# Performance work log

Measured on AMD Instinct MI355X. Metric: run time of the kernel, lower is better.

The kernel has to match this reference:

```python
import jax, jax.numpy as jnp
import numpy as np

NUM_NODES = 16
HSZ = 512
BSZ = 2048


def setup_inputs() -> dict:
    key = jax.random.key(0)
    ks = jax.random.split(key, 5)
    s = 0.02
    return {
        "graphs": jax.random.normal(ks[0], (BSZ, NUM_NODES, HSZ), dtype=jnp.float32),
        "W1": jax.random.normal(ks[1], (NUM_NODES, HSZ, HSZ), dtype=jnp.float32) * s,
        "b1": jnp.zeros((NUM_NODES, HSZ), dtype=jnp.float32),
        "W2": jax.random.normal(ks[2], (NUM_NODES, HSZ, HSZ), dtype=jnp.float32) * s,
        "b2": jnp.zeros((NUM_NODES, HSZ), dtype=jnp.float32),
        "Wg": jax.random.normal(ks[3], (NUM_NODES * HSZ, NUM_NODES), dtype=jnp.float32) * s,
        "bg": jnp.zeros((NUM_NODES,), dtype=jnp.float32),
    }


def reference(graphs, W1, b1, W2, b2, Wg, bg):
    bsz, num_nodes, hsz = graphs.shape
    # Per-node expert MLPs as one batched GEMM over the node axis (fused form
    # of the Python loop over ExpertModel instances).
    h = jax.nn.relu(jnp.einsum('bni,nih->bnh', graphs, W1) + b1)  # (bsz, n, hid)
    outs = jnp.einsum('bnh,nho->bno', h, W2) + b2                 # (bsz, n, out=hsz)
    # torch.cat(outputs, dim=-1).view(bsz, hsz, num_nodes): a raw reshape of the
    # concatenated (bsz, num_nodes*hsz) buffer -- NOT a transpose. Keep it faithful.
    cat = outs.reshape(bsz, num_nodes * hsz).reshape(bsz, hsz, num_nodes)
    # Gating over the flattened graph
    logits = graphs.reshape(bsz, num_nodes * hsz) @ Wg + bg       # (bsz, n)
    expert_probs = jax.nn.softmax(logits, axis=-1)[:, None, :]    # (bsz, 1, n)
    combined = (expert_probs * cat).sum(axis=-1)                  # (bsz, hsz)
    return combined, expert_probs
```

## Files before the change

### kernel.cpp

```cpp
#include <hip/hip_runtime.h>
#include <hip/hip_bf16.h>


typedef __attribute__((ext_vector_type(8))) short bf16x8;
typedef __attribute__((ext_vector_type(4))) float f32x4;

#define OFF_W1T  (0u)
#define OFF_W2T  (8388608u)
#define OFF_H    (16777216u)
#define OFF_PART (50331648u)
#define OFF_PROB (52428800u)
#define OFF_GB   (52559872u)
#define WS_NEED_NEW (86114304ull)

__device__ __forceinline__ void gl2lds16(const void* g, void* l) {
  __builtin_amdgcn_global_load_lds(
      (const __attribute__((address_space(1))) void*)g,
      (__attribute__((address_space(3))) void*)l, 16, 0, 0);
}

__device__ __forceinline__ void cvt16v(const float* __restrict__ src,
                                       bf16x8& lo, bf16x8& hi) {
  float f[16];
  *(float4*)(f + 0)  = *(const float4*)(src + 0);
  *(float4*)(f + 4)  = *(const float4*)(src + 4);
  *(float4*)(f + 8)  = *(const float4*)(src + 8);
  *(float4*)(f + 12) = *(const float4*)(src + 12);
  __hip_bfloat16 t[16];
#pragma unroll
  for (int e = 0; e < 16; e++) t[e] = __float2bfloat16(f[e]);
  lo = *(const bf16x8*)t;
  hi = *(const bf16x8*)(t + 8);
}

__device__ __forceinline__ void decode_bid(int bid, int& nblk, int& mblk, int& n) {
  int x8 = bid & 7;
  nblk = (bid >> 3) & 3;
  int pair = (bid >> 5) * 8 + x8;
  mblk = pair >> 4;
  n = pair & 15;
}

__global__ __launch_bounds__(256, 3) void prep_kernel(
    const float* __restrict__ graphs,
    const float* __restrict__ Wg,
    const float* __restrict__ W1, const float* __restrict__ W2,
    __hip_bfloat16* __restrict__ W1t, __hip_bfloat16* __restrict__ W2t,
    __hip_bfloat16* __restrict__ gb,
    float* __restrict__ partial) {
  __shared__ char smem[49664];
  const int tid = threadIdx.x, lane = tid & 63, wave = tid >> 6;

  if (blockIdx.x >= 1024) {
    const int t = blockIdx.x - 1024;
    const int bx = t & 63, by = t >> 6;
    const int ht = bx & 7, kt = bx >> 3;
    const int n = by & 15;
    const float* src = (by >> 4) ? W2 : W1;
    __hip_bfloat16* dst = (by >> 4) ? W2t : W1t;
    src += (size_t)n * 262144;
    dst += (size_t)n * 262144;
    const int hq4 = (tid & 15) * 4, kr = tid >> 4;
#pragma unroll
    for (int rr = 0; rr < 4; rr++) {
      const int kl = rr * 16 + kr;
      float4 v = *(const float4*)(src + (size_t)(kt * 64 + kl) * 512 + ht * 64 + hq4);
      __hip_bfloat16 t4[4] = {__float2bfloat16(v.x), __float2bfloat16(v.y),
                              __float2bfloat16(v.z), __float2bfloat16(v.w)};
#pragma unroll
      for (int i = 0; i < 4; i++)
        *(__hip_bfloat16*)(smem + (hq4 + i) * 144 + kl * 2) = t4[i];
    }
    __syncthreads();
    const int c8 = tid & 7, hr = tid >> 3;
#pragma unroll
    for (int rr = 0; rr < 2; rr++) {
      const int hl = rr * 32 + hr;
      bf16x8 v = *(const bf16x8*)(smem + hl * 144 + c8 * 16);
      *(bf16x8*)(dst + (size_t)(ht * 64 + hl) * 512 + kt * 64 + c8 * 8) = v;
    }
    return;
  }

  const int q = lane >> 4, l15 = lane & 15;
  const int n = blockIdx.x & 15, rb = blockIdx.x >> 4;
  char* Bt = smem + 33024;
  char* Aw = smem + wave * 8256;

  const int arow = lane >> 1, ahalf = (lane & 1) * 16;
  const float* Ag = graphs + (size_t)(rb * 32) * 8192 + n * 512 + wave * 128;

  float g[64];
  {
    const float* ap = Ag + (size_t)arow * 8192 + ahalf;
#pragma unroll
    for (int ks = 0; ks < 4; ks++)
#pragma unroll
      for (int j = 0; j < 4; j++)
        *(float4*)(g + ks * 16 + j * 4) = *(const float4*)(ap + ks * 32 + j * 4);
  }

#pragma unroll
  for (int i = 0; i < 2; i++) {
    int k = i * 256 + tid;
    const float* wr_ = Wg + (size_t)(n * 512 + k) * 16;
    float f[16];
    *(float4*)(f + 0)  = *(const float4*)(wr_ + 0);
    *(float4*)(f + 4)  = *(const float4*)(wr_ + 4);
    *(float4*)(f + 8)  = *(const float4*)(wr_ + 8);
    *(float4*)(f + 12) = *(const float4*)(wr_ + 12);
#pragma unroll
    for (int j = 0; j < 16; j++)
      *(__hip_bfloat16*)(Bt + j * 1040 + k * 2) = __float2bfloat16(f[j]);
  }
  __syncthreads();

  f32x4 acc[2] = {};
#pragma unroll
  for (int ks = 0; ks < 4; ks++) {
    const float* gc = g + ks * 16;
    __hip_bfloat16 t[16];
#pragma unroll
    for (int e = 0; e < 16; e++) t[e] = __float2bfloat16(gc[e]);
    bf16x8 lo = *(const bf16x8*)t, hi = *(const bf16x8*)(t + 8);
    const int c0 = ks * 4 + (lane & 1) * 2;
    const int rx = arow & 7;
    *(bf16x8*)(Aw + arow * 256 + ((c0 ^ rx) * 16)) = lo;
    *(bf16x8*)(Aw + arow * 256 + (((c0 + 1) ^ rx) * 16)) = hi;
    bf16x8 bv = *(const bf16x8*)(Bt + l15 * 1040 + (wave * 128 + ks * 32 + q * 8) * 2);
#pragma unroll
    for (int im = 0; im < 2; im++) {
      const int ar = im * 16 + l15;
      bf16x8 av = *(const bf16x8*)(Aw + ar * 256 + (((ks * 4 + q) ^ (ar & 7)) * 16));
      acc[im] = __builtin_amdgcn_mfma_f32_16x16x32_bf16(av, bv, acc[im], 0, 0, 0);
    }
  }
  __syncthreads();

#pragma unroll
  for (int im = 0; im < 2; im++)
#pragma unroll
    for (int r = 0; r < 4; r++)
      *(float*)(smem + 33024 + wave * 2048 + (im * 16 + q * 4 + r) * 64 + l15 * 4) = acc[im][r];

  __hip_bfloat16* gbase = gb + (size_t)(rb * 32) * 8192 + n * 512;
#pragma unroll
  for (int r = 0; r < 8; r++) {
    int u = r * 256 + tid;
    int row = u >> 6, cu = u & 63;
    int ch = (cu & 15) ^ (row & 7);
    bf16x8 v = *(const bf16x8*)(smem + (cu >> 4) * 8256 + row * 256 + ch * 16);
    *(bf16x8*)(gbase + (size_t)row * 8192 + cu * 8) = v;
  }
  __syncthreads();

#pragma unroll
  for (int i = 0; i < 2; i++) {
    int c = i * 256 + tid;
    int rrow = c >> 4, j = c & 15;
    float s = 0.f;
#pragma unroll
    for (int w = 0; w < 4; w++)
      s += *(const float*)(smem + 33024 + w * 2048 + rrow * 64 + j * 4);
    partial[((size_t)n * 2048 + rb * 32 + rrow) * 16 + j] = s;
  }
}

__global__ __launch_bounds__(256, 4) void gemm1_sm_kernel(
    const __hip_bfloat16* __restrict__ gbuf,
    const __hip_bfloat16* __restrict__ W1t,
    const float* __restrict__ b1,
    const float* __restrict__ partial,
    const float* __restrict__ bg,
    __hip_bfloat16* __restrict__ h,
    float* __restrict__ probs,
    float* __restrict__ probs_out) {
  __shared__ char smem[36864];
  const int tid = threadIdx.x, lane = tid & 63, wave = tid >> 6;

  if (blockIdx.x >= 1024) {
    const int r = (blockIdx.x - 1024) * 256 + tid;
    float s[16];
#pragma unroll
    for (int j = 0; j < 16; j++) s[j] = 0.f;
    for (int nn = 0; nn < 16; nn++) {
      const float4* p = (const float4*)(partial + ((size_t)nn * 2048 + r) * 16);
#pragma unroll
      for (int c = 0; c < 4; c++) {
        float4 v = p[c];
        s[c * 4 + 0] += v.x; s[c * 4 + 1] += v.y;
        s[c * 4 + 2] += v.z; s[c * 4 + 3] += v.w;
      }
    }
    float mx = -1e30f;
#pragma unroll
    for (int j = 0; j < 16; j++) { s[j] += bg[j]; mx = fmaxf(mx, s[j]); }
    float sum = 0.f;
#pragma unroll
    for (int j = 0; j < 16; j++) { s[j] = __expf(s[j] - mx); sum += s[j]; }
    float inv = 1.f / sum;
#pragma unroll
    for (int j = 0; j < 16; j++) s[j] *= inv;
    float4* pw = (float4*)(probs + (size_t)r * 16);
    float4* ow = (float4*)(probs_out + (size_t)r * 16);
#pragma unroll
    for (int c = 0; c < 4; c++) {
      float4 v = make_float4(s[c*4], s[c*4+1], s[c*4+2], s[c*4+3]);
      pw[c] = v; ow[c] = v;
    }
    return;
  }

  int nblk, mblk, n;
  decode_bid(blockIdx.x, nblk, mblk, n);
  const int wm = (wave >> 1) * 64, wn = (wave & 1) * 64;
  const int q = lane >> 4, l15 = lane & 15;
  const int lrow = lane >> 3, lcol = lane & 7;
  const int swz = (lcol ^ lrow) * 8;
  const int xr = l15 & 7;

  const __hip_bfloat16* Ag = gbuf + (size_t)(mblk * 128) * 8192 + n * 512;
  const __hip_bfloat16* Bg = W1t + (size_t)n * 262144 + (size_t)(nblk * 128) * 512;

  f32x4 acc[4][4] = {};
  for (int ks = 0; ks < 8; ks++) {
    const int k0 = ks * 64;
#pragma unroll
    for (int i = 0; i < 4; i++) {
      const int r = i * 32 + wave * 8 + lrow;
      gl2lds16(Ag + (size_t)r * 8192 + k0 + swz, smem + i * 4096 + wave * 1024 + lane * 16);
      gl2lds16(Bg + (size_t)r * 512 + k0 + swz,
               smem + 16384 + i * 4096 + wave * 1024 + lane * 16);
    }
    __syncthreads();
#pragma unroll
    for (int hh = 0; hh < 2; hh++) {
      const int co = ((q + hh * 4) ^ xr) * 16;
      bf16x8 av[4], bv[4];
#pragma unroll
      for (int im = 0; im < 4; im++)
        av[im] = *(const bf16x8*)(smem + (wm + im * 16 + l15) * 128 + co);
#pragma unroll
      for (int in = 0; in < 4; in++)
        bv[in] = *(const bf16x8*)(smem + 16384 + (wn + in * 16 + l15) * 128 + co);
#pragma unroll
      for (int im = 0; im < 4; im++)
#pragma unroll
        for (int in = 0; in < 4; in++)
          acc[im][in] = __builtin_amdgcn_mfma_f32_16x16x32_bf16(av[im], bv[in], acc[im][in], 0, 0, 0);
    }
    __syncthreads();
  }

  float bias[4];
#pragma unroll
  for (int in = 0; in < 4; in++)
    bias[in] = b1[n * 512 + nblk * 128 + wn + in * 16 + l15];
  char* epi = smem + wave * 9216;
#pragma unroll
  for (int im = 0; im < 4; im++)
#pragma unroll
    for (int in = 0; in < 4; in++)
#pragma unroll
      for (int r = 0; r < 4; r++) {
        float v = acc[im][in][r] + bias[in];
        v = fmaxf(v, 0.f);
        int rl = im * 16 + q * 4 + r;
        int cl = in * 16 + l15;
        *(__hip_bfloat16*)(epi + rl * 144 + cl * 2) = __float2bfloat16(v);
      }
  __syncthreads();
  __hip_bfloat16* Hg = h + (size_t)(mblk * 128 + wm) * 8192 + n * 512 + nblk * 128 + wn;
#pragma unroll
  for (int it = 0; it < 8; it++) {
    int rl = it * 8 + (lane >> 3);
    int cl = (lane & 7) * 8;
    bf16x8 v = *(const bf16x8*)(epi + rl * 144 + cl * 2);
    *(bf16x8*)(Hg + (size_t)rl * 8192 + cl) = v;
  }
}

__global__ __launch_bounds__(256) void transpose_kernel(
    const float* __restrict__ W1, const float* __restrict__ W2,
    __hip_bfloat16* __restrict__ W1t, __hip_bfloat16* __restrict__ W2t) {
  __shared__ char smem[9216];
  const int bx = blockIdx.x;
  const int ht = bx & 7, kt = bx >> 3;
  const int n = blockIdx.y & 15;
  const float* src = (blockIdx.y >> 4) ? W2 : W1;
  __hip_bfloat16* dst = (blockIdx.y >> 4) ? W2t : W1t;
  src += (size_t)n * 262144;
  dst += (size_t)n * 262144;
  const int tid = threadIdx.x;
  const int hq4 = (tid & 15) * 4, kr = tid >> 4;
#pragma unroll
  for (int rr = 0; rr < 4; rr++) {
    const int kl = rr * 16 + kr;
    float4 v = *(const float4*)(src + (size_t)(kt * 64 + kl) * 512 + ht * 64 + hq4);
    __hip_bfloat16 t4[4] = {__float2bfloat16(v.x), __float2bfloat16(v.y),
                            __float2bfloat16(v.z), __float2bfloat16(v.w)};
#pragma unroll
    for (int i = 0; i < 4; i++)
      *(__hip_bfloat16*)(smem + (hq4 + i) * 144 + kl * 2) = t4[i];
  }
  __syncthreads();
  const int c8 = tid & 7, hr = tid >> 3;
#pragma unroll
  for (int rr = 0; rr < 2; rr++) {
    const int hl = rr * 32 + hr;
    bf16x8 v = *(const bf16x8*)(smem + hl * 144 + c8 * 16);
    *(bf16x8*)(dst + (size_t)(ht * 64 + hl) * 512 + kt * 64 + c8 * 8) = v;
  }
}

__global__ void softmax_kernel(const float* __restrict__ partial,
                               const float* __restrict__ bg,
                               float* __restrict__ probs,
                               float* __restrict__ probs_out) {
  const int r = blockIdx.x * 256 + threadIdx.x;
  float s[16];
#pragma unroll
  for (int j = 0; j < 16; j++) s[j] = 0.f;
  for (int nn = 0; nn < 16; nn++) {
    const float4* p = (const float4*)(partial + ((size_t)nn * 2048 + r) * 16);
#pragma unroll
    for (int c = 0; c < 4; c++) {
      float4 v = p[c];
      s[c * 4 + 0] += v.x; s[c * 4 + 1] += v.y;
      s[c * 4 + 2] += v.z; s[c * 4 + 3] += v.w;
    }
  }
  float mx = -1e30f;
#pragma unroll
  for (int j = 0; j < 16; j++) { s[j] += bg[j]; mx = fmaxf(mx, s[j]); }
  float sum = 0.f;
#pragma unroll
  for (int j = 0; j < 16; j++) { s[j] = __expf(s[j] - mx); sum += s[j]; }
  float inv = 1.f / sum;
#pragma unroll
  for (int j = 0; j < 16; j++) s[j] *= inv;
  float4* pw = (float4*)(probs + (size_t)r * 16);
  float4* ow = (float4*)(probs_out + (size_t)r * 16);
#pragma unroll
  for (int c = 0; c < 4; c++) {
    float4 v = make_float4(s[c*4], s[c*4+1], s[c*4+2], s[c*4+3]);
    pw[c] = v; ow[c] = v;
  }
}

__global__ __launch_bounds__(256, 4) void gemm1_gate_kernel(
    const float* __restrict__ graphs,
    const __hip_bfloat16* __restrict__ W1t,
    const float* __restrict__ Wg,
    const float* __restrict__ b1,
    __hip_bfloat16* __restrict__ h,
    float* __restrict__ partial) {
  __shared__ char smem[36864];
  const int tid = threadIdx.x, lane = tid & 63, wave = tid >> 6;
  const int q = lane >> 4, l15 = lane & 15;

  if (blockIdx.x >= 1024) {
    const int gbid = blockIdx.x - 1024;
    const int n = gbid & 15, rb = gbid >> 4;
    char* Bt = smem + 8192;
#pragma unroll
    for (int i = 0; i < 2; i++) {
      int k = i * 256 + tid;
      const float* wr_ = Wg + (size_t)(n * 512 + k) * 16;
      float f[16];
      *(float4*)(f + 0)  = *(const float4*)(wr_ + 0);
      *(float4*)(f + 4)  = *(const float4*)(wr_ + 4);
      *(float4*)(f + 8)  = *(const float4*)(wr_ + 8);
      *(float4*)(f + 12) = *(const float4*)(wr_ + 12);
#pragma unroll
      for (int j = 0; j < 16; j++)
        *(__hip_bfloat16*)(Bt + j * 1040 + k * 2) = __float2bfloat16(f[j]);
    }
    __syncthreads();

    const int arow = lane >> 1, ahalf = (lane & 1) * 16;
    const float* Ag = graphs + (size_t)(rb * 32) * 8192 + n * 512 + wave * 128;
    char* Aw = smem + wave * 2048;

    f32x4 acc[2] = {};
    for (int ks = 0; ks < 4; ks++) {
      bf16x8 lo, hi;
      cvt16v(Ag + (size_t)arow * 8192 + ks * 32 + ahalf, lo, hi);
      char* d = Aw + arow * 64 + ahalf * 2;
      *(bf16x8*)d = lo;
      *(bf16x8*)(d + 16) = hi;
      bf16x8 bv = *(const bf16x8*)(Bt + l15 * 1040 + (wave * 128 + ks * 32 + q * 8) * 2);
#pragma unroll
      for (int im = 0; im < 2; im++) {
        bf16x8 av = *(const bf16x8*)(Aw + (im * 16 + l15) * 64 + q * 16);
        acc[im] = __builtin_amdgcn_mfma_f32_16x16x32_bf16(av, bv, acc[im], 0, 0, 0);
      }
    }
#pragma unroll
    for (int im = 0; im < 2; im++)
#pragma unroll
      for (int r = 0; r < 4; r++)
        *(float*)(smem + wave * 2048 + (im * 16 + q * 4 + r) * 64 + l15 * 4) = acc[im][r];
    __syncthreads();
#pragma unroll
    for (int i = 0; i < 2; i++) {
      int c = i * 256 + tid;
      int rrow = c >> 4, j = c & 15;
      float s = 0.f;
#pragma unroll
      for (int w = 0; w < 4; w++) s += *(const float*)(smem + w * 2048 + rrow * 64 + j * 4);
      partial[((size_t)n * 2048 + rb * 32 + rrow) * 16 + j] = s;
    }
    return;
  }

  int nblk, mblk, n;
  decode_bid(blockIdx.x, nblk, mblk, n);
  const int wm = (wave >> 1) * 64, wn = (wave & 1) * 64;
  const int lrow = lane >> 3, lcol = lane & 7;
  const int swz = (lcol ^ lrow) * 8;
  const int xr = l15 & 7;
  const int arow = tid >> 1, ahalf = (tid & 1) * 32;
  const int arx = arow & 7;

  const float* Ag = graphs + (size_t)(mblk * 128) * 8192 + n * 512;
  const __hip_bfloat16* Bg = W1t + (size_t)n * 262144 + (size_t)(nblk * 128) * 512;

  f32x4 acc[4][4] = {};
  for (int ks = 0; ks < 8; ks++) {
    const int k0 = ks * 64;
    const float* asrc = Ag + (size_t)arow * 8192 + k0 + ahalf;
    float f[32];
#pragma unroll
    for (int j = 0; j < 8; j++) *(float4*)(f + j * 4) = *(const float4*)(asrc + j * 4);
#pragma unroll
    for (int i = 0; i < 4; i++) {
      const int r = i * 32 + wave * 8 + lrow;
      gl2lds16(Bg + (size_t)r * 512 + k0 + swz,
               smem + 16384 + i * 4096 + wave * 1024 + lane * 16);
    }
    __hip_bfloat16 t[32];
#pragma unroll
    for (int e = 0; e < 32; e++) t[e] = __float2bfloat16(f[e]);
    char* abase = smem + arow * 128;
#pragma unroll
    for (int j = 0; j < 4; j++) {
      int c = (ahalf >> 3) + j;
      *(bf16x8*)(abase + ((c ^ arx) * 16)) = *(const bf16x8*)(t + j * 8);
    }
    __syncthreads();
#pragma unroll
    for (int hh = 0; hh < 2; hh++) {
      const int co = ((q + hh * 4) ^ xr) * 16;
      bf16x8 av[4], bv[4];
#pragma unroll
      for (int im = 0; im < 4; im++)
        av[im] = *(const bf16x8*)(smem + (wm + im * 16 + l15) * 128 + co);
#pragma unroll
      for (int in = 0; in < 4; in++)
        bv[in] = *(const bf16x8*)(smem + 16384 + (wn + in * 16 + l15) * 128 + co);
#pragma unroll
      for (int im = 0; im < 4; im++)
#pragma unroll
        for (int in = 0; in < 4; in++)
          acc[im][in] = __builtin_amdgcn_mfma_f32_16x16x32_bf16(av[im], bv[in], acc[im][in], 0, 0, 0);
    }
    __syncthreads();
  }

  float bias[4];
#pragma unroll
  for (int in = 0; in < 4; in++)
    bias[in] = b1[n * 512 + nblk * 128 + wn + in * 16 + l15];
  char* epi = smem + wave * 9216;
#pragma unroll
  for (int im = 0; im < 4; im++)
#pragma unroll
    for (int in = 0; in < 4; in++)
#pragma unroll
      for (int r = 0; r < 4; r++) {
        float v = acc[im][in][r] + bias[in];
        v = fmaxf(v, 0.f);
        int rl = im * 16 + q * 4 + r;
        int cl = in * 16 + l15;
        *(__hip_bfloat16*)(epi + rl * 144 + cl * 2) = __float2bfloat16(v);
      }
  __syncthreads();
  __hip_bfloat16* Hg = h + (size_t)(mblk * 128 + wm) * 8192 + n * 512 + nblk * 128 + wn;
#pragma unroll
  for (int it = 0; it < 8; it++) {
    int rl = it * 8 + (lane >> 3);
    int cl = (lane & 7) * 8;
    bf16x8 v = *(const bf16x8*)(epi + rl * 144 + cl * 2);
    *(bf16x8*)(Hg + (size_t)rl * 8192 + cl) = v;
  }
}

__global__ __launch_bounds__(256, 4) void gemm2_kernel(
    const __hip_bfloat16* __restrict__ hbuf,
    const __hip_bfloat16* __restrict__ W2t,
    const float* __restrict__ b2,
    const float* __restrict__ probs,
    float* __restrict__ out) {
  __shared__ char smem[32768];
  const int tid = threadIdx.x, lane = tid & 63, wave = tid >> 6;
  int nblk, mblk, n;
  decode_bid(blockIdx.x, nblk, mblk, n);
  const int wm = (wave >> 1) * 64, wn = (wave & 1) * 64;
  const int q = lane >> 4, l15 = lane & 15;
  const int lrow = lane >> 3, lcol = lane & 7;
  const int swz = (lcol ^ lrow) * 8;
  const int xr = l15 & 7;

  const __hip_bfloat16* Ag = hbuf + (size_t)(mblk * 128) * 8192 + n * 512;
  const __hip_bfloat16* Bg = W2t + (size_t)n * 262144 + (size_t)(nblk * 128) * 512;

  f32x4 acc[4][4] = {};
  for (int ks = 0; ks < 8; ks++) {
    const int k0 = ks * 64;
#pragma unroll
    for (int i = 0; i < 4; i++) {
      const int r = i * 32 + wave * 8 + lrow;
      gl2lds16(Ag + (size_t)r * 8192 + k0 + swz, smem + i * 4096 + wave * 1024 + lane * 16);
      gl2lds16(Bg + (size_t)r * 512 + k0 + swz,
               smem + 16384 + i * 4096 + wave * 1024 + lane * 16);
    }
    __syncthreads();
#pragma unroll
    for (int hh = 0; hh < 2; hh++) {
      const int co = ((q + hh * 4) ^ xr) * 16;
      bf16x8 av[4], bv[4];
#pragma unroll
      for (int im = 0; im < 4; im++)
        av[im] = *(const bf16x8*)(smem + (wm + im * 16 + l15) * 128 + co);
#pragma unroll
      for (int in = 0; in < 4; in++)
        bv[in] = *(const bf16x8*)(smem + 16384 + (wn + in * 16 + l15) * 128 + co);
#pragma unroll
      for (int im = 0; im < 4; im++)
#pragma unroll
        for (int in = 0; in < 4; in++)
          acc[im][in] = __builtin_amdgcn_mfma_f32_16x16x32_bf16(av[im], bv[in], acc[im][in], 0, 0, 0);
    }
    __syncthreads();
  }

  float bias[4];
#pragma unroll
  for (int in = 0; in < 4; in++)
    bias[in] = b2[n * 512 + nblk * 128 + wn + in * 16 + l15];
  float* comb = (float*)smem;
#pragma unroll
  for (int im = 0; im < 4; im++)
#pragma unroll
    for (int r = 0; r < 4; r++) {
      int rl = wm + im * 16 + q * 4 + r;
      float pv = probs[(size_t)(mblk * 128 + rl) * 16 + l15];
#pragma unroll
      for (int in = 0; in < 4; in++) {
        float v = (acc[im][in][r] + bias[in]) * pv;
        v += __shfl_xor(v, 1);
        v += __shfl_xor(v, 2);
        v += __shfl_xor(v, 4);
        v += __shfl_xor(v, 8);
        if (l15 == 0) comb[rl * 8 + (wn >> 4) + in] = v;
      }
    }
  __syncthreads();
  if (tid < 128) {
    float4 v0 = *(const float4*)(comb + tid * 8);
    float4 v1 = *(const float4*)(comb + tid * 8 + 4);
    float* orow = out + (size_t)(mblk * 128 + tid) * 512 + n * 32 + nblk * 8;
    *(float4*)orow = v0;
    *(float4*)(orow + 4) = v1;
  }
}

extern "C" void kernel_launch(void* const* d_in, const int* in_sizes, int n_in,
                              void* d_out, int out_size, void* d_ws, size_t ws_size,
                              hipStream_t stream) {
  const float* graphs = (const float*)d_in[0];
  const float* W1 = (const float*)d_in[1];
  const float* b1 = (const float*)d_in[2];
  const float* W2 = (const float*)d_in[3];
  const float* b2 = (const float*)d_in[4];
  const float* Wg = (const float*)d_in[5];
  const float* bg = (const float*)d_in[6];
  float* out = (float*)d_out;

  char* ws = (char*)d_ws;
  __hip_bfloat16* W1t = (__hip_bfloat16*)(ws + OFF_W1T);
  __hip_bfloat16* W2t = (__hip_bfloat16*)(ws + OFF_W2T);
  __hip_bfloat16* hb  = (__hip_bfloat16*)(ws + OFF_H);
  float* partial = (float*)(ws + OFF_PART);
  float* probs   = (float*)(ws + OFF_PROB);

  if (ws_size >= WS_NEED_NEW) {
    __hip_bfloat16* gbb = (__hip_bfloat16*)(ws + OFF_GB);
    prep_kernel<<<3072, 256, 0, stream>>>(graphs, Wg, W1, W2, W1t, W2t, gbb, partial);
    gemm1_sm_kernel<<<1032, 256, 0, stream>>>(gbb, W1t, b1, partial, bg, hb,
                                              probs, out + 2048 * 512);
  } else {
    transpose_kernel<<<dim3(64, 32), 256, 0, stream>>>(W1, W2, W1t, W2t);
    gemm1_gate_kernel<<<2048, 256, 0, stream>>>(graphs, W1t, Wg, b1, hb, partial);
    softmax_kernel<<<8, 256, 0, stream>>>(partial, bg, probs, out + 2048 * 512);
  }
  gemm2_kernel<<<1024, 256, 0, stream>>>(hb, W2t, b2, probs, out);
}
```

Measured before the change: 190.3 us.

## Add 256x256-tile second GEMM with 512-thread blocks and fused gating epilogue

Adds a new second-stage GEMM kernel that computes a 256x256 output tile per 512-thread workgroup with double-buffered LDS staging (128 KB shared memory), replacing the earlier 1024-block launch on the main workspace path. The epilogue applies bias and gating probabilities and reduces across the 16 interleaved columns with shuffles before writing the combined output. Larger tiles raise operand reuse per LDS load and cut the number of blocks, but the grid shrinks to 256 workgroups, which may leave compute units underused and limits occupancy because of the large LDS footprint.

```diff
diff --git a/kernel.cpp b/kernel.cpp
--- a/kernel.cpp
+++ b/kernel.cpp
@@ -277,6 +277,98 @@
     int cl = (lane & 7) * 8;
     bf16x8 v = *(const bf16x8*)(epi + rl * 144 + cl * 2);
     *(bf16x8*)(Hg + (size_t)rl * 8192 + cl) = v;
+  }
+}
+
+__global__ __launch_bounds__(512, 2) void gemm2_256_kernel(
+    const __hip_bfloat16* __restrict__ hbuf,
+    const __hip_bfloat16* __restrict__ W2t,
+    const float* __restrict__ b2,
+    const float* __restrict__ probs,
+    float* __restrict__ out) {
+  __shared__ char smem[131072];
+  const int tid = threadIdx.x, lane = tid & 63, wave = tid >> 6;
+  const int wgid = (blockIdx.x & 7) * 32 + (blockIdx.x >> 3);
+  const int n = wgid >> 4;
+  const int inner = wgid & 15;
+  const int mblk = inner >> 1, nblk2 = inner & 1;
+  const int wm = (wave >> 2) * 128;
+  const int wn = (wave & 3) * 64;
+  const int q = lane >> 4, l15 = lane & 15;
+  const int lrow = lane >> 3, lcol = lane & 7;
+  const int swz = (lcol ^ lrow) * 8;
+  const int xr = l15 & 7;
+
+  const __hip_bfloat16* Ag = hbuf + (size_t)(mblk * 256) * 8192 + n * 512;
+  const __hip_bfloat16* Bg = W2t + (size_t)n * 262144 + (size_t)(nblk2 * 256) * 512;
+
+  f32x4 acc[8][4] = {};
+
+  auto STAGE = [&](int b, int k0) {
+    char* Ab = smem + b * 65536;
+    char* Bb = Ab + 32768;
+#pragma unroll
+    for (int i = 0; i < 4; i++) {
+      const int r = i * 64 + wave * 8 + lrow;
+      gl2lds16(Ag + (size_t)r * 8192 + k0 + swz, Ab + i * 8192 + wave * 1024 + lane * 16);
+      gl2lds16(Bg + (size_t)r * 512 + k0 + swz, Bb + i * 8192 + wave * 1024 + lane * 16);
+    }
+  };
+
+  STAGE(0, 0);
+  __syncthreads();
+  for (int kt = 0; kt < 8; kt++) {
+    const int buf = kt & 1;
+    if (kt < 7) STAGE(buf ^ 1, (kt + 1) * 64);
+    const char* Ab = smem + buf * 65536;
+    const char* Bb = Ab + 32768;
+#pragma unroll
+    for (int hh = 0; hh < 2; hh++) {
+      const int co = ((q + hh * 4) ^ xr) * 16;
+      bf16x8 av[8], bv[4];
+#pragma unroll
+      for (int im = 0; im < 8; im++)
+        av[im] = *(const bf16x8*)(Ab + (wm + im * 16 + l15) * 128 + co);
+#pragma unroll
+      for (int in = 0; in < 4; in++)
+        bv[in] = *(const bf16x8*)(Bb + (wn + in * 16 + l15) * 128 + co);
+#pragma unroll
+      for (int im = 0; im < 8; im++)
+#pragma unroll
+        for (int in = 0; in < 4; in++)
+          acc[im][in] = __builtin_amdgcn_mfma_f32_16x16x32_bf16(av[im], bv[in], acc[im][in], 0, 0, 0);
+    }
+    __syncthreads();
+  }
+
+  float bias[4];
+#pragma unroll
+  for (int in = 0; in < 4; in++)
+    bias[in] = b2[n * 512 + nblk2 * 256 + wn + in * 16 + l15];
+  float* comb = (float*)smem;
+#pragma unroll
+  for (int im = 0; im < 8; im++)
+#pragma unroll
+    for (int r = 0; r < 4; r++) {
+      const int rl = wm + im * 16 + q * 4 + r;
+      float pv = probs[(size_t)(mblk * 256 + rl) * 16 + l15];
+#pragma unroll
+      for (int in = 0; in < 4; in++) {
+        float v = (acc[im][in][r] + bias[in]) * pv;
+        v += __shfl_xor(v, 1);
+        v += __shfl_xor(v, 2);
+        v += __shfl_xor(v, 4);
+        v += __shfl_xor(v, 8);
+        if (l15 == 0) comb[rl * 16 + (wn >> 4) + in] = v;
+      }
+    }
+  __syncthreads();
+#pragma unroll
+  for (int rnd = 0; rnd < 2; rnd++) {
+    const int idx = rnd * 512 + tid;
+    const int row = idx >> 2, c4 = idx & 3;
+    float4 v = *(const float4*)(comb + row * 16 + c4 * 4);
+    *(float4*)(out + (size_t)(mblk * 256 + row) * 512 + n * 32 + nblk2 * 16 + c4 * 4) = v;
   }
 }
 
@@ -600,10 +692,11 @@
     prep_kernel<<<3072, 256, 0, stream>>>(graphs, Wg, W1, W2, W1t, W2t, gbb, partial);
     gemm1_sm_kernel<<<1032, 256, 0, stream>>>(gbb, W1t, b1, partial, bg, hb,
                                               probs, out + 2048 * 512);
+    gemm2_256_kernel<<<256, 512, 0, stream>>>(hb, W2t, b2, probs, out);
   } else {
     transpose_kernel<<<dim3(64, 32), 256, 0, stream>>>(W1, W2, W1t, W2t);
     gemm1_gate_kernel<<<2048, 256, 0, stream>>>(graphs, W1t, Wg, b1, hb, partial);
     softmax_kernel<<<8, 256, 0, stream>>>(partial, bg, probs, out + 2048 * 512);
-  }
-  gemm2_kernel<<<1024, 256, 0, stream>>>(hb, W2t, b2, probs, out);
-}
+    gemm2_kernel<<<1024, 256, 0, stream>>>(hb, W2t, b2, probs, out);
+  }
+}
```

After: 198.4 us. +4.3%, slower.
